# Kernel optimization log

Hardware: AMD Instinct MI355X
Metric: run time of the kernel (lower is better)

The kernel has to match this reference:

```python
import jax, jax.numpy as jnp
import numpy as np

D_MODEL = 2048
N_HEADS = 16
HEAD_DIM = D_MODEL // N_HEADS
ROPE_BASE = 10000.0
B, T = 2, 2048


def setup_inputs() -> dict:
    key = jax.random.key(0)
    k1, k2, k3 = jax.random.split(key, 3)
    s_in = 1.0 / np.sqrt(D_MODEL)
    x = jax.random.normal(k1, (B, T, D_MODEL), dtype=jnp.float32)
    Wqkv = jax.random.normal(k2, (3 * D_MODEL, D_MODEL), dtype=jnp.float32) * s_in
    bqkv = jnp.zeros((3 * D_MODEL,), dtype=jnp.float32)
    Wo = jax.random.normal(k3, (D_MODEL, D_MODEL), dtype=jnp.float32) * s_in
    bo = jnp.zeros((D_MODEL,), dtype=jnp.float32)
    return {"x": x, "Wqkv": Wqkv, "bqkv": bqkv, "Wo": Wo, "bo": bo}


def _rotate_half(x):
    # [x1,x2,x3,x4] -> [-x2,x1,-x4,x3] (interleaved pairs)
    x_even = x[..., 0::2]
    x_odd = x[..., 1::2]
    return jnp.stack((-x_odd, x_even), axis=-1).reshape(x.shape)


def _rope_cos_sin(seq_len, dtype):
    half = HEAD_DIM // 2
    inv_freq = 1.0 / (ROPE_BASE ** (jnp.arange(half, dtype=jnp.float32) / half))
    freqs = jnp.arange(seq_len, dtype=jnp.float32)[:, None] * inv_freq[None, :]  # (T, half)
    emb = jnp.repeat(freqs, 2, axis=-1)  # (T, D) interleaved
    cos = jnp.cos(emb).astype(dtype)[None, None]  # (1,1,T,D)
    sin = jnp.sin(emb).astype(dtype)[None, None]
    return cos, sin


def reference(x, Wqkv, bqkv, Wo, bo):
    b, t, c = x.shape
    qkv = jnp.einsum('btc,fc->btf', x, Wqkv) + bqkv  # (B,T,3C)
    q, k, v = jnp.split(qkv, 3, axis=-1)
    def to_heads(z):
        return z.reshape(b, t, N_HEADS, HEAD_DIM).transpose(0, 2, 1, 3)  # (B,H,T,D)
    q, k, v = to_heads(q), to_heads(k), to_heads(v)
    cos, sin = _rope_cos_sin(t, x.dtype)
    q = q * cos + _rotate_half(q) * sin
    k = k * cos + _rotate_half(k) * sin
    scale = 1.0 / jnp.sqrt(jnp.asarray(HEAD_DIM, dtype=x.dtype))
    scores = jnp.einsum('bhqd,bhkd->bhqk', q, k) * scale  # (B,H,T,T)
    causal = jnp.tril(jnp.ones((t, t), dtype=bool))
    scores = jnp.where(causal, scores, jnp.finfo(scores.dtype).min)
    attn = jax.nn.softmax(scores, axis=-1)
    out = jnp.einsum('bhqk,bhkd->bhqd', attn, v)  # (B,H,T,D)
    out = out.transpose(0, 2, 1, 3).reshape(b, t, c)
    return jnp.einsum('btc,oc->bto', out, Wo) + bo
```

## Files before the change

### kernel.cpp

```cpp
#include <hip/hip_runtime.h>

using f16 = _Float16;
typedef _Float16 h8 __attribute__((ext_vector_type(8)));
typedef _Float16 h4 __attribute__((ext_vector_type(4)));
typedef float f4 __attribute__((ext_vector_type(4)));
typedef unsigned int u32;
typedef unsigned long long u64;

#define DEVI static __device__ __forceinline__

DEVI f4 mfma16(h8 a, h8 b, f4 c) {
  return __builtin_amdgcn_mfma_f32_16x16x32_f16(a, b, c, 0, 0, 0);
}

DEVI void gl_lds16(const f16* g, f16* l) {
  __builtin_amdgcn_global_load_lds(
      (const __attribute__((address_space(1))) u32*)g,
      (__attribute__((address_space(3))) u32*)l, 16, 0, 0);
}

DEVI u32 pkh2(float a, float b) {
  union { f16 h[2]; u32 u; } x;
  x.h[0] = (f16)a; x.h[1] = (f16)b;
  return x.u;
}

typedef float fv4 __attribute__((ext_vector_type(4)));

__global__ __launch_bounds__(256) void k_cvt(const float* __restrict__ in,
                                             f16* __restrict__ out, int n4) {
  int i = blockIdx.x * 256 + threadIdx.x;
  if (i >= n4) return;
  fv4 v = ((const fv4*)in)[i];
  h4 o;
  o[0] = (f16)v[0]; o[1] = (f16)v[1]; o[2] = (f16)v[2]; o[3] = (f16)v[3];
  ((h4*)out)[i] = o;
}

__global__ __launch_bounds__(256) void k_rope_tbl(float* __restrict__ tbl) {
  int i = blockIdx.x * 256 + threadIdx.x;
  int t = i >> 6, d = i & 63;
  float invf = exp2f(-(float)d * (13.287712379549449f / 64.f));
  float a = (float)t * invf;
  tbl[2 * i]     = cosf(a);
  tbl[2 * i + 1] = sinf(a);
}

template <int F32OUT>
__global__ __launch_bounds__(512, 2) void k_gemm256(const f16* __restrict__ A,
                                                    const f16* __restrict__ Bt,
                                                    const float* __restrict__ bias,
                                                    void* __restrict__ Cp,
                                                    int M, int N, int K, int gy) {
  __shared__ f16 lds[2][24576];
  const int tid = threadIdx.x;
  const int w = tid >> 6, lane = tid & 63;
  const int g = lane >> 4, colq = lane & 15;
  const int wr = w >> 2, wc = w & 3;

  const int nwg = gridDim.x;
  const int q8 = nwg >> 3;
  const int swz = (blockIdx.x & 7) * q8 + (blockIdx.x >> 3);
  const int bm = swz % gy, bn = swz / gy;

  const f16* Ab = A + (size_t)bm * 128 * K;
  const f16* Bb = Bt + (size_t)bn * 256 * K;

  const int srow = lane >> 3;
  const int schunk = (lane & 7) ^ srow;
  const int nt = K >> 6;

  auto STAGE = [&](int kt, f16* buf) {
    const int k0 = kt << 6;
    f16* bA = buf;
    f16* bB = buf + 128 * 64;
#pragma unroll
    for (int j = 0; j < 2; ++j) {
      const int r = w * 16 + j * 8;
      gl_lds16(Ab + (size_t)(r + srow) * K + k0 + schunk * 8, bA + r * 64);
    }
#pragma unroll
    for (int j = 0; j < 4; ++j) {
      const int r = w * 32 + j * 8;
      gl_lds16(Bb + (size_t)(r + srow) * K + k0 + schunk * 8, bB + r * 64);
    }
  };

  STAGE(0, lds[0]);
  STAGE(1, lds[1]);
  asm volatile("s_waitcnt vmcnt(6)" ::: "memory");
  __builtin_amdgcn_s_barrier();

  f4 acc[4][4] = {};
  const int rowA0 = wr * 64 + colq;
  const int rowB0 = wc * 64 + colq;
  const int cq7 = colq & 7;

  for (int t = 0; t < nt; ++t) {
    f16* cur = lds[t & 1];
    h8 af[2][4], bf[2][4];
#pragma unroll
    for (int kki = 0; kki < 2; ++kki) {
#pragma unroll
      for (int m = 0; m < 4; ++m)
        af[kki][m] = *(const h8*)(cur + (rowA0 + m * 16) * 64 + (((kki * 4 + g) ^ cq7) * 8));
#pragma unroll
      for (int n = 0; n < 4; ++n)
        bf[kki][n] = *(const h8*)(cur + 8192 + (rowB0 + n * 16) * 64 + (((kki * 4 + g) ^ cq7) * 8));
    }
    asm volatile("s_waitcnt lgkmcnt(0)" ::: "memory");
    __builtin_amdgcn_s_barrier();
    const bool more = (t + 2 < nt);
    if (more) STAGE(t + 2, cur);
    __builtin_amdgcn_s_setprio(1);
#pragma unroll
    for (int m = 0; m < 4; ++m)
#pragma unroll
      for (int n = 0; n < 4; ++n)
#pragma unroll
        for (int kki = 0; kki < 2; ++kki)
          acc[m][n] = mfma16(af[kki][m], bf[kki][n], acc[m][n]);
    __builtin_amdgcn_s_setprio(0);
    if (more) {
      asm volatile("s_waitcnt vmcnt(6)" ::: "memory");
    } else {
      asm volatile("s_waitcnt vmcnt(0)" ::: "memory");
    }
    __builtin_amdgcn_s_barrier();
  }

#pragma unroll
  for (int n = 0; n < 4; ++n) {
    const int col = bn * 256 + wc * 64 + n * 16 + colq;
    const float bv = bias[col];
#pragma unroll
    for (int m = 0; m < 4; ++m) {
      const int row0 = bm * 128 + wr * 64 + m * 16 + 4 * g;
#pragma unroll
      for (int r = 0; r < 4; ++r) {
        float v = acc[m][n][r] + bv;
        if constexpr (F32OUT) {
          ((float*)Cp)[(size_t)(row0 + r) * N + col] = v;
        } else {
          ((f16*)Cp)[(size_t)(row0 + r) * N + col] = (f16)v;
        }
      }
    }
  }
}

__global__ __launch_bounds__(256) void k_rope(const f16* __restrict__ qkv,
                                              const float* __restrict__ tbl,
                                              f16* __restrict__ Q, f16* __restrict__ K) {
  int i = blockIdx.x * 256 + threadIdx.x;
  int d = i & 63;
  int h = (i >> 6) & 15;
  int bt = i >> 10;
  int t = bt & 2047;
  int bh = ((bt >> 11) << 4) | h;
  union { u32 u; f16 h2[2]; } qa, ka, qo, ko;
  qa.u = *(const u32*)(qkv + (size_t)bt * 6144 + h * 128 + 2 * d);
  ka.u = *(const u32*)(qkv + (size_t)bt * 6144 + 2048 + h * 128 + 2 * d);
  float c = tbl[2 * (t * 64 + d)];
  float s = tbl[2 * (t * 64 + d) + 1];
  float q0f = (float)qa.h2[0], q1f = (float)qa.h2[1];
  float k0f = (float)ka.h2[0], k1f = (float)ka.h2[1];
  const float SQ = 0.088388347648318447f * 1.4426950408889634f;
  qo.h2[0] = (f16)((q0f * c - q1f * s) * SQ);
  qo.h2[1] = (f16)((q1f * c + q0f * s) * SQ);
  ko.h2[0] = (f16)(k0f * c - k1f * s);
  ko.h2[1] = (f16)(k1f * c + k0f * s);
  *(u32*)(Q + ((size_t)bh * 2048 + t) * 128 + 2 * d) = qo.u;
  *(u32*)(K + ((size_t)bh * 2048 + t) * 128 + 2 * d) = ko.u;
}

__global__ __launch_bounds__(256) void k_vtrans(const f16* __restrict__ qkv,
                                                f16* __restrict__ Vt) {
  __shared__ f16 ldsT[128 * 40];
  const int bh = blockIdx.y, t0 = blockIdx.x * 32;
  const int b = bh >> 4, h = bh & 15;
  const int tid = threadIdx.x;
#pragma unroll
  for (int cc = 0; cc < 2; ++cc) {
    int task = tid + cc * 256;
    int row = task >> 4;
    int ch = task & 15;
    h8 v = *(const h8*)(qkv + (size_t)(b * 2048 + t0 + row) * 6144 + 4096 + h * 128 + ch * 8);
#pragma unroll
    for (int j = 0; j < 8; ++j) ldsT[(ch * 8 + j) * 40 + row] = v[j];
  }
  __syncthreads();
  int d = tid >> 1, seg = tid & 1;
  h8 v0 = *(const h8*)(ldsT + d * 40 + seg * 16);
  h8 v1 = *(const h8*)(ldsT + d * 40 + seg * 16 + 8);
  f16* dst = Vt + ((size_t)bh * 128 + d) * 2048 + t0 + seg * 16;
  *(h8*)dst = v0;
  *(h8*)(dst + 8) = v1;
}

DEVI void stage_tiles(const f16* __restrict__ Kg, const f16* __restrict__ Vtg,
                      f16* bufK, f16* bufV, int kv, int w, int lane) {
#pragma unroll
  for (int jj = 0; jj < 4; ++jj) {
    const int j = w * 4 + jj;
    const int rK = j * 4 + (lane >> 4);
    const int cK = (lane & 15) ^ ((rK & 7) << 1);
    gl_lds16(Kg + (size_t)(kv + rK) * 128 + cK * 8, bufK + j * 512);
    const int rV = j * 8 + (lane >> 3);
    const int cV = (lane & 7) ^ (rV & 7);
    gl_lds16(Vtg + (size_t)rV * 2048 + kv + cV * 8, bufV + j * 512);
  }
}

__global__ __launch_bounds__(256, 1) void k_attn(const f16* __restrict__ Q,
                                                 const f16* __restrict__ K,
                                                 const f16* __restrict__ Vt,
                                                 f16* __restrict__ O) {
  __shared__ f16 lds[2][16384];
  const int tid = threadIdx.x;
  const int w = tid >> 6, lane = tid & 63;
  const int g = lane >> 4, q = lane & 15;
  const int bid = blockIdx.x;
  const int bh = bid & 31;
  const int b = bid >> 5;

  const f16* Kg = K + (size_t)bh * 2048 * 128;
  const f16* Vtg = Vt + (size_t)bh * 128 * 2048;
  const int qx2 = (q & 7) << 1;
  const int qx = q & 7;

  for (int ph = 0; ph < 2; ++ph) {
    const int p = ph ? (15 - b) : b;
    const int q0w = p * 128 + w * 32;
    const int nit = 2 * (p + 1);

    h8 qf[2][4];
#pragma unroll
    for (int set = 0; set < 2; ++set)
#pragma unroll
      for (int d4 = 0; d4 < 4; ++d4)
        qf[set][d4] = *(const h8*)(Q + ((size_t)bh * 2048 + q0w + 16 * set + q) * 128 + d4 * 32 + g * 8);

    stage_tiles(Kg, Vtg, lds[0], lds[0] + 8192, 0, w, lane);
    asm volatile("s_waitcnt vmcnt(0)" ::: "memory");
    __builtin_amdgcn_s_barrier();

    f4 ot[2][8] = {};
    float mrun[2] = {-3.0e38f, -3.0e38f};
    float lrun[2] = {0.f, 0.f};

    for (int it = 0; it < nit; ++it) {
      const int kv0 = it * 64;
      f16* bufK = lds[it & 1];
      f16* bufV = bufK + 8192;
      if (it + 1 < nit) {
        f16* nb = lds[(it + 1) & 1];
        stage_tiles(Kg, Vtg, nb, nb + 8192, kv0 + 64, w, lane);
      }
      if (kv0 < q0w + 32) {
        f4 st[2][4] = {{{0.f,0.f,0.f,0.f},{0.f,0.f,0.f,0.f},{0.f,0.f,0.f,0.f},{0.f,0.f,0.f,0.f}},
                       {{0.f,0.f,0.f,0.f},{0.f,0.f,0.f,0.f},{0.f,0.f,0.f,0.f},{0.f,0.f,0.f,0.f}}};
#pragma unroll
        for (int d4 = 0; d4 < 4; ++d4) {
          h8 kf[4];
#pragma unroll
          for (int s = 0; s < 4; ++s)
            kf[s] = *(const h8*)(bufK + ((16 * s + q) * 16 + ((4 * d4 + g) ^ qx2)) * 8);
#pragma unroll
          for (int set = 0; set < 2; ++set)
#pragma unroll
            for (int s = 0; s < 4; ++s)
              st[set][s] = mfma16(kf[s], qf[set][d4], st[set][s]);
        }
        if (kv0 + 63 > q0w) {
#pragma unroll
          for (int set = 0; set < 2; ++set) {
            const int qcol = q0w + 16 * set + q;
#pragma unroll
            for (int s = 0; s < 4; ++s)
#pragma unroll
              for (int r = 0; r < 4; ++r)
                if (kv0 + s * 16 + 4 * g + r > qcol) st[set][s][r] = -3.0e38f;
          }
        }
        float pm[2];
#pragma unroll
        for (int set = 0; set < 2; ++set) {
          float m0 = st[set][0][0];
#pragma unroll
          for (int s = 0; s < 4; ++s)
#pragma unroll
            for (int r = 0; r < 4; ++r) m0 = fmaxf(m0, st[set][s][r]);
          m0 = fmaxf(m0, __shfl_xor(m0, 16));
          m0 = fmaxf(m0, __shfl_xor(m0, 32));
          pm[set] = m0;
        }
        const bool ok = (pm[0] <= mrun[0] + 8.0f) && (pm[1] <= mrun[1] + 8.0f);
        if (!__all(ok)) {
#pragma unroll
          for (int set = 0; set < 2; ++set) {
            float mnew = fmaxf(mrun[set], pm[set]);
            float corr = exp2f(mrun[set] - mnew);
            lrun[set] *= corr;
#pragma unroll
            for (int dt = 0; dt < 8; ++dt) ot[set][dt] *= corr;
            mrun[set] = mnew;
          }
        }
#pragma unroll
        for (int set = 0; set < 2; ++set) {
          float ps = 0.f;
#pragma unroll
          for (int s = 0; s < 4; ++s)
#pragma unroll
            for (int r = 0; r < 4; ++r) {
              st[set][s][r] = exp2f(st[set][s][r] - mrun[set]);
              ps += st[set][s][r];
            }
          ps += __shfl_xor(ps, 16);
          ps += __shfl_xor(ps, 32);
          lrun[set] += ps;
        }
        union { u32 u[4]; h8 h; } pb[2][2];
        const int s0l = ((g & 1) << 5) | q;
        const bool hi = g >= 2;
#pragma unroll
        for (int set = 0; set < 2; ++set)
#pragma unroll
          for (int hh = 0; hh < 2; ++hh) {
            u32 wA0 = pkh2(st[set][2 * hh][0], st[set][2 * hh][1]);
            u32 wB0 = pkh2(st[set][2 * hh][2], st[set][2 * hh][3]);
            u32 wA1 = pkh2(st[set][2 * hh + 1][0], st[set][2 * hh + 1][1]);
            u32 wB1 = pkh2(st[set][2 * hh + 1][2], st[set][2 * hh + 1][3]);
            u32 a0 = (u32)__shfl((int)wA0, s0l),      a1 = (u32)__shfl((int)wA1, s0l);
            u32 b0 = (u32)__shfl((int)wB0, s0l),      b1 = (u32)__shfl((int)wB1, s0l);
            u32 c0 = (u32)__shfl((int)wA0, s0l + 16), c1 = (u32)__shfl((int)wA1, s0l + 16);
            u32 d0 = (u32)__shfl((int)wB0, s0l + 16), d1 = (u32)__shfl((int)wB1, s0l + 16);
            pb[set][hh].u[0] = hi ? a1 : a0;
            pb[set][hh].u[1] = hi ? b1 : b0;
            pb[set][hh].u[2] = hi ? c1 : c0;
            pb[set][hh].u[3] = hi ? d1 : d0;
          }
#pragma unroll
        for (int hh = 0; hh < 2; ++hh)
#pragma unroll
          for (int dt = 0; dt < 8; ++dt) {
            h8 vf = *(const h8*)(bufV + ((dt * 16 + q) * 8 + ((4 * hh + g) ^ qx)) * 8);
#pragma unroll
            for (int set = 0; set < 2; ++set)
              ot[set][dt] = mfma16(vf, pb[set][hh].h, ot[set][dt]);
          }
      }
      asm volatile("s_waitcnt vmcnt(0)" ::: "memory");
      __builtin_amdgcn_s_barrier();
    }

#pragma unroll
    for (int set = 0; set < 2; ++set) {
      float linv = 1.0f / lrun[set];
      f16* Ob = O + ((size_t)(bh >> 4) * 2048 + q0w + 16 * set + q) * 2048 + (bh & 15) * 128 + 4 * g;
#pragma unroll
      for (int dt = 0; dt < 8; ++dt) {
        union { f16 hh4[4]; u64 u; } o;
#pragma unroll
        for (int r = 0; r < 4; ++r) o.hh4[r] = (f16)(ot[set][dt][r] * linv);
        *(u64*)(Ob + dt * 16) = o.u;
      }
    }
  }
}

extern "C" void kernel_launch(void* const* d_in, const int* in_sizes, int n_in,
                              void* d_out, int out_size, void* d_ws, size_t ws_size,
                              hipStream_t stream) {
  (void)in_sizes; (void)n_in; (void)out_size; (void)ws_size;
  const float* x    = (const float*)d_in[0];
  const float* Wqkv = (const float*)d_in[1];
  const float* bqkv = (const float*)d_in[2];
  const float* Wo   = (const float*)d_in[3];
  const float* bo   = (const float*)d_in[4];

  char* ws = (char*)d_ws;
  f16* xb    = (f16*)ws; ws += (size_t)4096 * 2048 * 2;
  f16* wqkvb = (f16*)ws; ws += (size_t)6144 * 2048 * 2;
  f16* wob   = (f16*)ws; ws += (size_t)2048 * 2048 * 2;
  f16* qkvb  = (f16*)ws; ws += (size_t)4096 * 6144 * 2;
  f16* Qb    = (f16*)ws; ws += (size_t)32 * 2048 * 128 * 2;
  f16* Kb    = (f16*)ws; ws += (size_t)32 * 2048 * 128 * 2;
  f16* Vtb   = (f16*)ws; ws += (size_t)32 * 128 * 2048 * 2;
  f16* attb  = (f16*)ws; ws += (size_t)4096 * 2048 * 2;
  float* tbl = (float*)ws; ws += (size_t)2048 * 64 * 2 * 4;

  k_cvt<<<8192, 256, 0, stream>>>(x, xb, 2097152);
  k_cvt<<<12288, 256, 0, stream>>>(Wqkv, wqkvb, 3145728);
  k_cvt<<<4096, 256, 0, stream>>>(Wo, wob, 1048576);
  k_rope_tbl<<<512, 256, 0, stream>>>(tbl);

  k_gemm256<0><<<768, 512, 0, stream>>>(xb, wqkvb, bqkv, qkvb, 4096, 6144, 2048, 32);

  k_rope<<<16384, 256, 0, stream>>>(qkvb, tbl, Qb, Kb);
  k_vtrans<<<dim3(64, 32), 256, 0, stream>>>(qkvb, Vtb);

  k_attn<<<256, 256, 0, stream>>>(Qb, Kb, Vtb, attb);

  k_gemm256<1><<<256, 512, 0, stream>>>(attb, wob, bo, d_out, 4096, 2048, 2048, 32);
}
```

Before: 317.9 us.

## Enlarge GEMM tiles to 256x256 with half-K staged four-phase pipeline

The shared GEMM kernel moves from 128x256 to 256x256 output tiles, so each wave now holds 8x4 accumulators. The K loop is split into 32-wide halves that are staged separately and interleaved with four MFMA sub-phases, using sched_barrier and extra s_barriers. The aim is more data reuse per LDS load and finer overlap of global-to-LDS copies with compute. In exchange, the XOR swizzle is dropped, and 64-byte row strides may cause LDS bank conflicts. LDS use doubles to 128 KB, so at most one block fits per CU, and the grids shrink to 384 and 128 blocks, which risks idle CUs and tail effects.

```diff
diff --git a/kernel.cpp b/kernel.cpp
--- a/kernel.cpp
+++ b/kernel.cpp
@@ -52,7 +52,7 @@
                                                     const float* __restrict__ bias,
                                                     void* __restrict__ Cp,
                                                     int M, int N, int K, int gy) {
-  __shared__ f16 lds[2][24576];
+  __shared__ f16 lds[2][32768];
   const int tid = threadIdx.x;
   const int w = tid >> 6, lane = tid & 63;
   const int g = lane >> 4, colq = lane & 15;
@@ -63,66 +63,100 @@
   const int swz = (blockIdx.x & 7) * q8 + (blockIdx.x >> 3);
   const int bm = swz % gy, bn = swz / gy;
 
-  const f16* Ab = A + (size_t)bm * 128 * K;
+  const f16* Ab = A + (size_t)bm * 256 * K;
   const f16* Bb = Bt + (size_t)bn * 256 * K;
-
-  const int srow = lane >> 3;
-  const int schunk = (lane & 7) ^ srow;
   const int nt = K >> 6;
 
-  auto STAGE = [&](int kt, f16* buf) {
-    const int k0 = kt << 6;
-    f16* bA = buf;
-    f16* bB = buf + 128 * 64;
+  const int srb = lane >> 2;
+  const int scc = (lane & 3) << 3;
+
+  auto STAGE_A = [&](int kt, int h, f16* buf) {
+    const int k0 = (kt << 6) + (h << 5);
 #pragma unroll
     for (int j = 0; j < 2; ++j) {
-      const int r = w * 16 + j * 8;
-      gl_lds16(Ab + (size_t)(r + srow) * K + k0 + schunk * 8, bA + r * 64);
-    }
-#pragma unroll
-    for (int j = 0; j < 4; ++j) {
-      const int r = w * 32 + j * 8;
-      gl_lds16(Bb + (size_t)(r + srow) * K + k0 + schunk * 8, bB + r * 64);
+      const int r = (w * 2 + j) * 16;
+      gl_lds16(Ab + (size_t)(r + srb) * K + k0 + scc, buf + h * 8192 + r * 32);
     }
   };
-
-  STAGE(0, lds[0]);
-  STAGE(1, lds[1]);
-  asm volatile("s_waitcnt vmcnt(6)" ::: "memory");
+  auto STAGE_B = [&](int kt, int h, f16* buf) {
+    const int k0 = (kt << 6) + (h << 5);
+#pragma unroll
+    for (int j = 0; j < 2; ++j) {
+      const int r = (w * 2 + j) * 16;
+      gl_lds16(Bb + (size_t)(r + srb) * K + k0 + scc, buf + 16384 + h * 8192 + r * 32);
+    }
+  };
+
+  f4 acc[8][4] = {};
+
+  auto LDA = [&](h8* dst, int mh, int h, const f16* cur) {
+#pragma unroll
+    for (int m = 0; m < 4; ++m)
+      dst[m] = *(const h8*)(cur + h * 8192 + (wr * 128 + (mh * 4 + m) * 16 + colq) * 32 + g * 8);
+  };
+  auto LDB = [&](h8* dst, int h, const f16* cur) {
+#pragma unroll
+    for (int n = 0; n < 4; ++n)
+      dst[n] = *(const h8*)(cur + 16384 + h * 8192 + (wc * 64 + n * 16 + colq) * 32 + g * 8);
+  };
+  auto MM = [&](h8* af, h8* bf, int mh) {
+#pragma unroll
+    for (int m = 0; m < 4; ++m)
+#pragma unroll
+      for (int n = 0; n < 4; ++n)
+        acc[mh * 4 + m][n] = mfma16(af[m], bf[n], acc[mh * 4 + m][n]);
+  };
+
+  STAGE_A(0, 0, lds[0]); STAGE_B(0, 0, lds[0]);
+  STAGE_A(0, 1, lds[0]); STAGE_B(0, 1, lds[0]);
+  STAGE_A(1, 0, lds[1]); STAGE_B(1, 0, lds[1]);
+  asm volatile("s_waitcnt vmcnt(4)" ::: "memory");
   __builtin_amdgcn_s_barrier();
-
-  f4 acc[4][4] = {};
-  const int rowA0 = wr * 64 + colq;
-  const int rowB0 = wc * 64 + colq;
-  const int cq7 = colq & 7;
 
   for (int t = 0; t < nt; ++t) {
     f16* cur = lds[t & 1];
-    h8 af[2][4], bf[2][4];
-#pragma unroll
-    for (int kki = 0; kki < 2; ++kki) {
-#pragma unroll
-      for (int m = 0; m < 4; ++m)
-        af[kki][m] = *(const h8*)(cur + (rowA0 + m * 16) * 64 + (((kki * 4 + g) ^ cq7) * 8));
-#pragma unroll
-      for (int n = 0; n < 4; ++n)
-        bf[kki][n] = *(const h8*)(cur + 8192 + (rowB0 + n * 16) * 64 + (((kki * 4 + g) ^ cq7) * 8));
-    }
+    f16* nxt = lds[(t & 1) ^ 1];
+    const bool m1 = (t + 1 < nt), m2 = (t + 2 < nt);
+    h8 af[4], bf[4];
+    LDA(af, 0, 0, cur);
+    LDB(bf, 0, cur);
+    if (m1) STAGE_A(t + 1, 1, nxt);
+    __builtin_amdgcn_s_barrier();
     asm volatile("s_waitcnt lgkmcnt(0)" ::: "memory");
-    __builtin_amdgcn_s_barrier();
-    const bool more = (t + 2 < nt);
-    if (more) STAGE(t + 2, cur);
+    __builtin_amdgcn_sched_barrier(0);
     __builtin_amdgcn_s_setprio(1);
-#pragma unroll
-    for (int m = 0; m < 4; ++m)
-#pragma unroll
-      for (int n = 0; n < 4; ++n)
-#pragma unroll
-        for (int kki = 0; kki < 2; ++kki)
-          acc[m][n] = mfma16(af[kki][m], bf[kki][n], acc[m][n]);
+    MM(af, bf, 0);
     __builtin_amdgcn_s_setprio(0);
-    if (more) {
-      asm volatile("s_waitcnt vmcnt(6)" ::: "memory");
+    __builtin_amdgcn_s_barrier();
+    LDA(af, 1, 0, cur);
+    if (m1) STAGE_B(t + 1, 1, nxt);
+    __builtin_amdgcn_s_barrier();
+    asm volatile("s_waitcnt lgkmcnt(0)" ::: "memory");
+    __builtin_amdgcn_sched_barrier(0);
+    __builtin_amdgcn_s_setprio(1);
+    MM(af, bf, 1);
+    __builtin_amdgcn_s_setprio(0);
+    __builtin_amdgcn_s_barrier();
+    LDA(af, 0, 1, cur);
+    LDB(bf, 1, cur);
+    if (m2) STAGE_A(t + 2, 0, cur);
+    __builtin_amdgcn_s_barrier();
+    asm volatile("s_waitcnt lgkmcnt(0)" ::: "memory");
+    __builtin_amdgcn_sched_barrier(0);
+    __builtin_amdgcn_s_setprio(1);
+    MM(af, bf, 0);
+    __builtin_amdgcn_s_setprio(0);
+    __builtin_amdgcn_s_barrier();
+    LDA(af, 1, 1, cur);
+    if (m2) STAGE_B(t + 2, 0, cur);
+    __builtin_amdgcn_s_barrier();
+    asm volatile("s_waitcnt lgkmcnt(0)" ::: "memory");
+    __builtin_amdgcn_sched_barrier(0);
+    __builtin_amdgcn_s_setprio(1);
+    MM(af, bf, 1);
+    __builtin_amdgcn_s_setprio(0);
+    if (m2) {
+      asm volatile("s_waitcnt vmcnt(4)" ::: "memory");
     } else {
       asm volatile("s_waitcnt vmcnt(0)" ::: "memory");
     }
@@ -134,8 +168,8 @@
     const int col = bn * 256 + wc * 64 + n * 16 + colq;
     const float bv = bias[col];
 #pragma unroll
-    for (int m = 0; m < 4; ++m) {
-      const int row0 = bm * 128 + wr * 64 + m * 16 + 4 * g;
+    for (int m = 0; m < 8; ++m) {
+      const int row0 = bm * 256 + wr * 128 + m * 16 + 4 * g;
 #pragma unroll
       for (int r = 0; r < 4; ++r) {
         float v = acc[m][n][r] + bv;
@@ -396,12 +430,12 @@
   k_cvt<<<4096, 256, 0, stream>>>(Wo, wob, 1048576);
   k_rope_tbl<<<512, 256, 0, stream>>>(tbl);
 
-  k_gemm256<0><<<768, 512, 0, stream>>>(xb, wqkvb, bqkv, qkvb, 4096, 6144, 2048, 32);
+  k_gemm256<0><<<384, 512, 0, stream>>>(xb, wqkvb, bqkv, qkvb, 4096, 6144, 2048, 16);
 
   k_rope<<<16384, 256, 0, stream>>>(qkvb, tbl, Qb, Kb);
   k_vtrans<<<dim3(64, 32), 256, 0, stream>>>(qkvb, Vtb);
 
   k_attn<<<256, 256, 0, stream>>>(Qb, Kb, Vtb, attb);
 
-  k_gemm256<1><<<256, 512, 0, stream>>>(attb, wob, bo, d_out, 4096, 2048, 2048, 32);
-}
+  k_gemm256<1><<<128, 512, 0, stream>>>(attb, wob, bo, d_out, 4096, 2048, 2048, 16);
+}
```

Result: slower. 349.9 us (+10.1%).

## Use single-buffered 128x128 GEMM tiles and fuse RoPE with V transpose

Applied to the files above, without the earlier changes.

Replaces the double-buffered 128x256 GEMM with a simpler 256-thread kernel that loads one 128x128 tile per k-step and synchronizes twice per iteration, doubling the grid size. It also merges the RoPE and V-transpose kernels into a single launch that handles Q/K rotation and V transposition per 32-token block. The aim is more workgroups and fewer launches, at the cost of losing load/compute overlap in the GEMM and halving B-tile reuse.

```diff
diff --git a/kernel.cpp b/kernel.cpp
--- a/kernel.cpp
+++ b/kernel.cpp
@@ -47,16 +47,17 @@
 }
 
 template <int F32OUT>
-__global__ __launch_bounds__(512, 2) void k_gemm256(const f16* __restrict__ A,
-                                                    const f16* __restrict__ Bt,
-                                                    const float* __restrict__ bias,
-                                                    void* __restrict__ Cp,
-                                                    int M, int N, int K, int gy) {
-  __shared__ f16 lds[2][24576];
+__global__ __launch_bounds__(256) void k_gemm97(const f16* __restrict__ A,
+                                                const f16* __restrict__ Bt,
+                                                const float* __restrict__ bias,
+                                                void* __restrict__ Cp,
+                                                int M, int N, int K, int gy) {
+  __shared__ f16 sA[128 * 64];
+  __shared__ f16 sB[128 * 64];
   const int tid = threadIdx.x;
   const int w = tid >> 6, lane = tid & 63;
   const int g = lane >> 4, colq = lane & 15;
-  const int wr = w >> 2, wc = w & 3;
+  const int wr = w >> 1, wc = w & 1;
 
   const int nwg = gridDim.x;
   const int q8 = nwg >> 3;
@@ -64,55 +65,36 @@
   const int bm = swz % gy, bn = swz / gy;
 
   const f16* Ab = A + (size_t)bm * 128 * K;
-  const f16* Bb = Bt + (size_t)bn * 256 * K;
+  const f16* Bb = Bt + (size_t)bn * 128 * K;
+  const int nt = K >> 6;
 
   const int srow = lane >> 3;
   const int schunk = (lane & 7) ^ srow;
-  const int nt = K >> 6;
-
-  auto STAGE = [&](int kt, f16* buf) {
-    const int k0 = kt << 6;
-    f16* bA = buf;
-    f16* bB = buf + 128 * 64;
-#pragma unroll
-    for (int j = 0; j < 2; ++j) {
-      const int r = w * 16 + j * 8;
-      gl_lds16(Ab + (size_t)(r + srow) * K + k0 + schunk * 8, bA + r * 64);
-    }
-#pragma unroll
-    for (int j = 0; j < 4; ++j) {
-      const int r = w * 32 + j * 8;
-      gl_lds16(Bb + (size_t)(r + srow) * K + k0 + schunk * 8, bB + r * 64);
-    }
-  };
-
-  STAGE(0, lds[0]);
-  STAGE(1, lds[1]);
-  asm volatile("s_waitcnt vmcnt(6)" ::: "memory");
-  __builtin_amdgcn_s_barrier();
+  const int cq7 = colq & 7;
 
   f4 acc[4][4] = {};
   const int rowA0 = wr * 64 + colq;
   const int rowB0 = wc * 64 + colq;
-  const int cq7 = colq & 7;
 
   for (int t = 0; t < nt; ++t) {
-    f16* cur = lds[t & 1];
+    const int k0 = t << 6;
+#pragma unroll
+    for (int j = 0; j < 4; ++j) {
+      const int r = (w * 4 + j) * 8;
+      gl_lds16(Ab + (size_t)(r + srow) * K + k0 + schunk * 8, sA + r * 64);
+      gl_lds16(Bb + (size_t)(r + srow) * K + k0 + schunk * 8, sB + r * 64);
+    }
+    __syncthreads();
     h8 af[2][4], bf[2][4];
 #pragma unroll
     for (int kki = 0; kki < 2; ++kki) {
 #pragma unroll
       for (int m = 0; m < 4; ++m)
-        af[kki][m] = *(const h8*)(cur + (rowA0 + m * 16) * 64 + (((kki * 4 + g) ^ cq7) * 8));
+        af[kki][m] = *(const h8*)(sA + (rowA0 + m * 16) * 64 + (((kki * 4 + g) ^ cq7) * 8));
 #pragma unroll
       for (int n = 0; n < 4; ++n)
-        bf[kki][n] = *(const h8*)(cur + 8192 + (rowB0 + n * 16) * 64 + (((kki * 4 + g) ^ cq7) * 8));
-    }
-    asm volatile("s_waitcnt lgkmcnt(0)" ::: "memory");
-    __builtin_amdgcn_s_barrier();
-    const bool more = (t + 2 < nt);
-    if (more) STAGE(t + 2, cur);
-    __builtin_amdgcn_s_setprio(1);
+        bf[kki][n] = *(const h8*)(sB + (rowB0 + n * 16) * 64 + (((kki * 4 + g) ^ cq7) * 8));
+    }
 #pragma unroll
     for (int m = 0; m < 4; ++m)
 #pragma unroll
@@ -120,18 +102,12 @@
 #pragma unroll
         for (int kki = 0; kki < 2; ++kki)
           acc[m][n] = mfma16(af[kki][m], bf[kki][n], acc[m][n]);
-    __builtin_amdgcn_s_setprio(0);
-    if (more) {
-      asm volatile("s_waitcnt vmcnt(6)" ::: "memory");
-    } else {
-      asm volatile("s_waitcnt vmcnt(0)" ::: "memory");
-    }
-    __builtin_amdgcn_s_barrier();
+    __syncthreads();
   }
 
 #pragma unroll
   for (int n = 0; n < 4; ++n) {
-    const int col = bn * 256 + wc * 64 + n * 16 + colq;
+    const int col = bn * 128 + wc * 64 + n * 16 + colq;
     const float bv = bias[col];
 #pragma unroll
     for (int m = 0; m < 4; ++m) {
@@ -149,33 +125,10 @@
   }
 }
 
-__global__ __launch_bounds__(256) void k_rope(const f16* __restrict__ qkv,
-                                              const float* __restrict__ tbl,
-                                              f16* __restrict__ Q, f16* __restrict__ K) {
-  int i = blockIdx.x * 256 + threadIdx.x;
-  int d = i & 63;
-  int h = (i >> 6) & 15;
-  int bt = i >> 10;
-  int t = bt & 2047;
-  int bh = ((bt >> 11) << 4) | h;
-  union { u32 u; f16 h2[2]; } qa, ka, qo, ko;
-  qa.u = *(const u32*)(qkv + (size_t)bt * 6144 + h * 128 + 2 * d);
-  ka.u = *(const u32*)(qkv + (size_t)bt * 6144 + 2048 + h * 128 + 2 * d);
-  float c = tbl[2 * (t * 64 + d)];
-  float s = tbl[2 * (t * 64 + d) + 1];
-  float q0f = (float)qa.h2[0], q1f = (float)qa.h2[1];
-  float k0f = (float)ka.h2[0], k1f = (float)ka.h2[1];
-  const float SQ = 0.088388347648318447f * 1.4426950408889634f;
-  qo.h2[0] = (f16)((q0f * c - q1f * s) * SQ);
-  qo.h2[1] = (f16)((q1f * c + q0f * s) * SQ);
-  ko.h2[0] = (f16)(k0f * c - k1f * s);
-  ko.h2[1] = (f16)(k1f * c + k0f * s);
-  *(u32*)(Q + ((size_t)bh * 2048 + t) * 128 + 2 * d) = qo.u;
-  *(u32*)(K + ((size_t)bh * 2048 + t) * 128 + 2 * d) = ko.u;
-}
-
-__global__ __launch_bounds__(256) void k_vtrans(const f16* __restrict__ qkv,
-                                                f16* __restrict__ Vt) {
+__global__ __launch_bounds__(256) void k_ropev(const f16* __restrict__ qkv,
+                                               const float* __restrict__ tbl,
+                                               f16* __restrict__ Q, f16* __restrict__ K,
+                                               f16* __restrict__ Vt) {
   __shared__ f16 ldsT[128 * 40];
   const int bh = blockIdx.y, t0 = blockIdx.x * 32;
   const int b = bh >> 4, h = bh & 15;
@@ -188,6 +141,28 @@
     h8 v = *(const h8*)(qkv + (size_t)(b * 2048 + t0 + row) * 6144 + 4096 + h * 128 + ch * 8);
 #pragma unroll
     for (int j = 0; j < 8; ++j) ldsT[(ch * 8 + j) * 40 + row] = v[j];
+  }
+  const float SQ = 0.088388347648318447f * 1.4426950408889634f;
+#pragma unroll
+  for (int cc = 0; cc < 8; ++cc) {
+    int task = tid + cc * 256;
+    int row = task >> 6;
+    int d = task & 63;
+    int t = t0 + row;
+    const f16* src = qkv + (size_t)(b * 2048 + t) * 6144 + h * 128 + 2 * d;
+    union { u32 u; f16 h2[2]; } qa, ka, qo, ko;
+    qa.u = *(const u32*)src;
+    ka.u = *(const u32*)(src + 2048);
+    float c = tbl[2 * (t * 64 + d)];
+    float s = tbl[2 * (t * 64 + d) + 1];
+    float q0f = (float)qa.h2[0], q1f = (float)qa.h2[1];
+    float k0f = (float)ka.h2[0], k1f = (float)ka.h2[1];
+    qo.h2[0] = (f16)((q0f * c - q1f * s) * SQ);
+    qo.h2[1] = (f16)((q1f * c + q0f * s) * SQ);
+    ko.h2[0] = (f16)(k0f * c - k1f * s);
+    ko.h2[1] = (f16)(k1f * c + k0f * s);
+    *(u32*)(Q + ((size_t)bh * 2048 + t) * 128 + 2 * d) = qo.u;
+    *(u32*)(K + ((size_t)bh * 2048 + t) * 128 + 2 * d) = ko.u;
   }
   __syncthreads();
   int d = tid >> 1, seg = tid & 1;
@@ -396,12 +371,11 @@
   k_cvt<<<4096, 256, 0, stream>>>(Wo, wob, 1048576);
   k_rope_tbl<<<512, 256, 0, stream>>>(tbl);
 
-  k_gemm256<0><<<768, 512, 0, stream>>>(xb, wqkvb, bqkv, qkvb, 4096, 6144, 2048, 32);
-
-  k_rope<<<16384, 256, 0, stream>>>(qkvb, tbl, Qb, Kb);
-  k_vtrans<<<dim3(64, 32), 256, 0, stream>>>(qkvb, Vtb);
+  k_gemm97<0><<<1536, 256, 0, stream>>>(xb, wqkvb, bqkv, qkvb, 4096, 6144, 2048, 32);
+
+  k_ropev<<<dim3(64, 32), 256, 0, stream>>>(qkvb, tbl, Qb, Kb, Vtb);
 
   k_attn<<<256, 256, 0, stream>>>(Qb, Kb, Vtb, attb);
 
-  k_gemm256<1><<<256, 512, 0, stream>>>(attb, wob, bo, d_out, 4096, 2048, 2048, 32);
-}
+  k_gemm97<1><<<512, 256, 0, stream>>>(attb, wob, bo, d_out, 4096, 2048, 2048, 32);
+}
```

After: 325.6 us. 1.02x slower.
